# Kernel tuning notes

Hardware: AMD Instinct MI355X
Metric: run time of the kernel (lower is better)

## Reference

```python
import math
import jax, jax.numpy as jnp
import numpy as np

TWO_PI = 2.0 * math.pi


def make_coords(H, W):
    """Replicates ConvNet.generate_coordinates -> offsets of shape (9, 2, H, W).
    Pair k gives (dy, dx) for kernel tap k (row-major 3x3); center tap (k=4) is zero."""
    gy, gx = jnp.meshgrid(jnp.arange(H, dtype=jnp.float32),
                          jnp.arange(W, dtype=jnp.float32), indexing='ij')
    cy = H / 2.0 - 0.5
    cx = W / 2.0 - 0.5
    # torch: delta_x along height, delta_y along width; theta = atan2(dy, dx) mod 2pi
    theta = jnp.arctan2(gx - cx, gy - cy) % TWO_PI
    theta = jnp.round(theta * 10000.0) / 10000.0
    # per-tap (angle multiple m of pi/4, additive (ay, ax)); tap 4 (center) stays zero
    taps = [(0, 1.0, 1.0), (1, 1.0, 0.0), (2, 1.0, -1.0), (3, 0.0, 1.0), None,
            (4, 0.0, -1.0), (5, -1.0, 1.0), (6, -1.0, 0.0), (7, -1.0, -1.0)]
    offs = []
    zero = jnp.zeros_like(theta)
    for t in taps:
        if t is None:
            offs.append(jnp.stack([zero, zero]))
        else:
            m, ay, ax = t
            ang = theta + (math.pi / 4.0) * m
            offs.append(jnp.stack([jnp.cos(ang) + ay, jnp.sin(ang) + ax]))
    return jnp.stack(offs)  # (9, 2, H, W)


def deform_conv(x, off, w):
    """torchvision.ops.deform_conv2d, 3x3, stride 1, pad 1, dilation 1, no bias.
    x: (B,C,H,W), off: (9,2,H,W), w: (O,C,3,3) -> (B,O,H,W)."""
    B, C, H, W = x.shape
    ky = jnp.repeat(jnp.arange(3, dtype=jnp.float32), 3)  # (9,)
    kx = jnp.tile(jnp.arange(3, dtype=jnp.float32), 3)
    # sampling positions (H, W, 9)
    py = (jnp.arange(H, dtype=jnp.float32)[:, None, None] - 1.0
          + ky[None, None, :] + jnp.transpose(off[:, 0], (1, 2, 0)))
    px = (jnp.arange(W, dtype=jnp.float32)[None, :, None] - 1.0
          + kx[None, None, :] + jnp.transpose(off[:, 1], (1, 2, 0)))
    y0 = jnp.floor(py)
    x0 = jnp.floor(px)
    wy = py - y0  # bilinear weights
    wx = px - x0

    def gather(yf, xf):
        valid = (yf >= 0) & (yf <= H - 1) & (xf >= 0) & (xf <= W - 1)
        yi = jnp.clip(yf, 0, H - 1).astype(jnp.int32)
        xi = jnp.clip(xf, 0, W - 1).astype(jnp.int32)
        return x[:, :, yi, xi] * valid.astype(x.dtype)  # (B,C,H,W,9)

    sampled = ((1 - wy) * (1 - wx) * gather(y0, x0)
               + (1 - wy) * wx * gather(y0, x0 + 1)
               + wy * (1 - wx) * gather(y0 + 1, x0)
               + wy * wx * gather(y0 + 1, x0 + 1))
    return jnp.einsum('bchwk,ock->bohw', sampled, w.reshape(w.shape[0], C, 9))


def maxpool2(x):
    B, C, H, W = x.shape
    return x.reshape(B, C, H // 2, 2, W // 2, 2).max(axis=(3, 5))


def setup_inputs() -> dict:
    key = jax.random.key(0)
    ks = jax.random.split(key, 20)

    def kaiming(k, shape):
        fan_in = int(np.prod(shape[1:]))
        return jax.random.normal(k, shape, jnp.float32) * np.float32(np.sqrt(2.0 / fan_in))

    inp = {'x': jax.random.normal(ks[0], (8, 3, 128, 128), jnp.float32)}
    conv_shapes = [('w11', (64, 3, 3, 3)), ('w12', (64, 64, 3, 3)),
                   ('w21', (128, 64, 3, 3)), ('w22', (128, 128, 3, 3)),
                   ('w31', (256, 128, 3, 3)), ('w32', (256, 256, 3, 3)), ('w33', (256, 256, 3, 3)),
                   ('w41', (512, 256, 3, 3)), ('w42', (512, 512, 3, 3)), ('w43', (512, 512, 3, 3)),
                   ('w51', (512, 512, 3, 3)), ('w52', (512, 512, 3, 3)), ('w53', (512, 512, 3, 3))]
    for i, (n, s) in enumerate(conv_shapes):
        inp[n] = kaiming(ks[i + 1], s)
    inp['fc1_w'] = kaiming(ks[14], (4096, 512))
    inp['fc1_b'] = jnp.zeros((4096,), jnp.float32)
    inp['fc2_w'] = kaiming(ks[15], (4096, 4096))
    inp['fc2_b'] = jnp.zeros((4096,), jnp.float32)
    inp['fc3_w'] = kaiming(ks[16], (30, 4096))
    inp['fc3_b'] = jnp.zeros((30,), jnp.float32)
    return inp


def reference(x, w11, w12, w21, w22, w31, w32, w33, w41, w42, w43,
              w51, w52, w53, fc1_w, fc1_b, fc2_w, fc2_b, fc3_w, fc3_b):
    c128 = make_coords(128, 128)
    c64 = make_coords(64, 64)
    c32 = make_coords(32, 32)
    c16 = make_coords(16, 16)
    c8 = make_coords(8, 8)
    r = jax.nn.relu
    x = r(deform_conv(x, c128, w11))
    x = r(deform_conv(x, c128, w12))
    x = maxpool2(x)
    x = r(deform_conv(x, c64, w21))
    x = r(deform_conv(x, c64, w22))
    x = maxpool2(x)
    x = r(deform_conv(x, c32, w31))
    x = r(deform_conv(x, c32, w32))
    x = r(deform_conv(x, c32, w33))
    x = maxpool2(x)
    x = r(deform_conv(x, c16, w41))
    x = r(deform_conv(x, c16, w42))
    x = r(deform_conv(x, c16, w43))
    x = maxpool2(x)
    x = r(deform_conv(x, c8, w51))
    x = r(deform_conv(x, c8, w52))
    x = r(deform_conv(x, c8, w53))
    x = maxpool2(x)          # -> (B, 512, 4, 4)
    x = x.mean(axis=(2, 3))  # AvgPool2d((4,4)) on 4x4 -> (B, 512)
    x = r(x @ fc1_w.T + fc1_b)
    x = r(x @ fc2_w.T + fc2_b)
    return x @ fc3_w.T + fc3_b  # (B, 30)
```

## Files before the change

kernel.cpp:

```cpp
#include <hip/hip_runtime.h>
#include <math.h>

#define TWO_PI_F 6.283185307179586f
#define PI_4_F   0.7853981633974483f

typedef __attribute__((ext_vector_type(8))) short short8;
typedef __attribute__((ext_vector_type(4))) float f32x4;
typedef __attribute__((ext_vector_type(2))) float f32x2;
typedef __attribute__((ext_vector_type(4))) unsigned short ushort4v;
typedef __attribute__((ext_vector_type(4))) unsigned int uint4v;
typedef __attribute__((ext_vector_type(2))) unsigned int uint2v;

struct Tap { int i00, i01, i10, i11; float w00, w01, w10, w11; };

static __device__ __forceinline__ unsigned short f2bf(float f) {
    unsigned u = __builtin_bit_cast(unsigned, f);
    u = (u + 0x7fffu + ((u >> 16) & 1u)) >> 16;
    return (unsigned short)u;
}
static __device__ __forceinline__ float bf2f(unsigned short u) {
    return __builtin_bit_cast(float, (unsigned)u << 16);
}
static __device__ __forceinline__ f32x2 up2(unsigned u) {
    f32x2 r;
    r.x = __builtin_bit_cast(float, u << 16);
    r.y = __builtin_bit_cast(float, u & 0xffff0000u);
    return r;
}
static __device__ __forceinline__ unsigned cvt_pk_bf16(float lo, float hi) {
    unsigned r;
    asm("v_cvt_pk_bf16_f32 %0, %1, %2" : "=v"(r) : "v"(lo), "v"(hi));
    return r;
}

__global__ void build_table_kernel(Tap* __restrict__ tab, int* __restrict__ tabA, int S) {
    int idx = blockIdx.x * blockDim.x + threadIdx.x;
    int total = S * S * 9;
    if (idx >= total) return;
    int k = idx % 9;
    int p = idx / 9;
    int y = p / S;
    int x = p - y * S;
    int HW = S * S;

    float c = 0.5f * (float)S - 0.5f;
    float theta = atan2f((float)x - c, (float)y - c);
    theta = fmodf(theta, TWO_PI_F);
    if (theta < 0.0f) theta += TWO_PI_F;
    theta = rintf(theta * 10000.0f) / 10000.0f;

    float offy = 0.0f, offx = 0.0f;
    if (k != 4) {
        int m = (k < 4) ? k : (k - 1);
        const float ayt[8] = { 1.f, 1.f,  1.f, 0.f,  0.f, -1.f, -1.f, -1.f };
        const float axt[8] = { 1.f, 0.f, -1.f, 1.f, -1.f,  1.f,  0.f, -1.f };
        float ang = theta + PI_4_F * (float)m;
        offy = cosf(ang) + ayt[m];
        offx = sinf(ang) + axt[m];
    }
    int ky = k / 3, kx = k - ky * 3;
    float py = (float)y - 1.0f + (float)ky + offy;
    float px = (float)x - 1.0f + (float)kx + offx;
    float fy0 = floorf(py), fx0 = floorf(px);
    float wy = py - fy0, wx = px - fx0;
    float fmaxc = (float)(S - 1);

    Tap t;
    {
        float yy = fy0, xx = fx0;
        bool v = (yy >= 0.f) && (yy <= fmaxc) && (xx >= 0.f) && (xx <= fmaxc);
        int yi = (int)fminf(fmaxf(yy, 0.f), fmaxc);
        int xi = (int)fminf(fmaxf(xx, 0.f), fmaxc);
        t.i00 = yi * S + xi;
        t.w00 = v ? (1.f - wy) * (1.f - wx) : 0.f;
    }
    {
        float yy = fy0, xx = fx0 + 1.0f;
        bool v = (yy >= 0.f) && (yy <= fmaxc) && (xx >= 0.f) && (xx <= fmaxc);
        int yi = (int)fminf(fmaxf(yy, 0.f), fmaxc);
        int xi = (int)fminf(fmaxf(xx, 0.f), fmaxc);
        t.i01 = yi * S + xi;
        t.w01 = v ? (1.f - wy) * wx : 0.f;
    }
    {
        float yy = fy0 + 1.0f, xx = fx0;
        bool v = (yy >= 0.f) && (yy <= fmaxc) && (xx >= 0.f) && (xx <= fmaxc);
        int yi = (int)fminf(fmaxf(yy, 0.f), fmaxc);
        int xi = (int)fminf(fmaxf(xx, 0.f), fmaxc);
        t.i10 = yi * S + xi;
        t.w10 = v ? wy * (1.f - wx) : 0.f;
    }
    {
        float yy = fy0 + 1.0f, xx = fx0 + 1.0f;
        bool v = (yy >= 0.f) && (yy <= fmaxc) && (xx >= 0.f) && (xx <= fmaxc);
        int yi = (int)fminf(fmaxf(yy, 0.f), fmaxc);
        int xi = (int)fminf(fmaxf(xx, 0.f), fmaxc);
        t.i11 = yi * S + xi;
        t.w11 = v ? wy * wx : 0.f;
    }
    tab[idx] = t;

    int rec = (k * HW + p) * 8;
    tabA[rec + 0] = t.i00;
    tabA[rec + 1] = t.i01;
    tabA[rec + 2] = t.i10;
    tabA[rec + 3] = t.i11;
    tabA[rec + 4] = __builtin_bit_cast(int, t.w00);
    tabA[rec + 5] = __builtin_bit_cast(int, t.w01);
    tabA[rec + 6] = __builtin_bit_cast(int, t.w10);
    tabA[rec + 7] = __builtin_bit_cast(int, t.w11);
}

__global__ void pack_w_kernel(const float* __restrict__ w, unsigned short* __restrict__ wP,
                              int O, int C, int total) {
    int idx = blockIdx.x * blockDim.x + threadIdx.x;
    if (idx >= total) return;
    int ksub = idx & 31;
    int kbo  = idx >> 5;
    int o  = kbo % O;
    int kb = kbo / O;
    int K = kb * 32 + ksub;
    int kt = K / C;
    int c  = K - kt * C;
    wP[idx] = f2bf(w[((size_t)o * C + c) * 9 + kt]);
}

__global__ __launch_bounds__(256) void dconv_f32_kernel(
    const float* __restrict__ x, const float* __restrict__ w,
    const Tap* __restrict__ tab, unsigned short* __restrict__ out,
    int C, int O, int HW)
{
    __shared__ float4 sTabRaw[64 * 9 * 2];
    __shared__ float  sS[9][64];
    __shared__ float  sW[9][64];

    const int tid = threadIdx.x;
    const int b  = blockIdx.z;
    const int o0 = blockIdx.y * 64;
    const int p0 = blockIdx.x * 64;
    const int C9 = C * 9;

    const float4* gt = (const float4*)(tab + (size_t)p0 * 9);
    for (int i = tid; i < 64 * 9 * 2; i += 256) sTabRaw[i] = gt[i];
    const Tap* sTab = (const Tap*)sTabRaw;
    __syncthreads();

    float acc[4][4];
#pragma unroll
    for (int i = 0; i < 4; ++i)
#pragma unroll
        for (int j = 0; j < 4; ++j) acc[i][j] = 0.f;

    const int to = tid >> 4;
    const int tn = tid & 15;
    const float* xb = x + (size_t)b * C * HW;

    for (int c = 0; c < C; ++c) {
        const float* xp = xb + (size_t)c * HW;
        for (int i = tid; i < 9 * 64; i += 256) {
            int k = i >> 6;
            int p = i & 63;
            Tap t = sTab[p * 9 + k];
            sS[k][p] = t.w00 * xp[t.i00] + t.w01 * xp[t.i01]
                     + t.w10 * xp[t.i10] + t.w11 * xp[t.i11];
        }
        for (int i = tid; i < 9 * 64; i += 256) {
            int k = i >> 6;
            int o = i & 63;
            sW[k][o] = w[(size_t)(o0 + o) * C9 + c * 9 + k];
        }
        __syncthreads();
#pragma unroll
        for (int k = 0; k < 9; ++k) {
            float4 wv = *(const float4*)&sW[k][to * 4];
            float4 sv = *(const float4*)&sS[k][tn * 4];
            acc[0][0] += wv.x * sv.x; acc[0][1] += wv.x * sv.y; acc[0][2] += wv.x * sv.z; acc[0][3] += wv.x * sv.w;
            acc[1][0] += wv.y * sv.x; acc[1][1] += wv.y * sv.y; acc[1][2] += wv.y * sv.z; acc[1][3] += wv.y * sv.w;
            acc[2][0] += wv.z * sv.x; acc[2][1] += wv.z * sv.y; acc[2][2] += wv.z * sv.z; acc[2][3] += wv.z * sv.w;
            acc[3][0] += wv.w * sv.x; acc[3][1] += wv.w * sv.y; acc[3][2] += wv.w * sv.z; acc[3][3] += wv.w * sv.w;
        }
        __syncthreads();
    }

    const int ob   = (o0 + to * 4) >> 3;
    const int osub = (to & 1) << 2;
#pragma unroll
    for (int j = 0; j < 4; ++j) {
        int p = p0 + tn * 4 + j;
        ushort4v v;
        v.x = f2bf(fmaxf(acc[0][j], 0.f));
        v.y = f2bf(fmaxf(acc[1][j], 0.f));
        v.z = f2bf(fmaxf(acc[2][j], 0.f));
        v.w = f2bf(fmaxf(acc[3][j], 0.f));
        *(ushort4v*)(out + (((size_t)b * (O >> 3) + ob) * HW + p) * 8 + osub) = v;
    }
}

#define SPITCH 296

template<int BM>
__global__ __launch_bounds__(256, 4) void dconv_mfma(
    const unsigned short* __restrict__ x, const unsigned short* __restrict__ wP,
    const int* __restrict__ tabA, unsigned short* __restrict__ out,
    float* __restrict__ part,
    int C, int O, int HW, int Cchunk, int nChunks)
{
    __shared__ unsigned short sS[64 * SPITCH];

    const int tid  = threadIdx.x;
    const int lane = tid & 63;
    const int wv   = tid >> 6;
    const int bz = blockIdx.z;
    const int b     = bz & 7;
    const int chunk = bz >> 3;

    int bx = blockIdx.x;
    const int gx = gridDim.x;
    if ((gx & 7) == 0) { int g8 = gx >> 3; bx = (bx & 7) * g8 + (bx >> 3); }

    const int o0 = blockIdx.y * BM;
    const int p0 = bx * 64;
    const int c0 = chunk * Cchunk;
    const int nGroups = Cchunk >> 5;

    const int o0w = (BM == 128) ? wv * 32 : (wv >> 1) * 32;
    const int p0w = (BM == 128) ? 0       : (wv & 1) * 32;
    constexpr int MF = 2;
    constexpr int NF = (BM == 128) ? 4 : 2;

    f32x4 acc[MF][NF] = {};

    const unsigned short* xb = x + (size_t)b * C * HW;
    const int quad = lane >> 4;
    const int l16  = lane & 15;
    const int* tq = tabA + (((size_t)(p0 + lane)) << 3);
    unsigned short* srow = &sS[lane * SPITCH + (wv << 3)];

    for (int g = 0; g < nGroups; ++g) {
        const int cg = c0 + g * 32;
        const unsigned short* xcb = xb + ((((size_t)(cg >> 3) + wv) * HW) << 3);

#pragma unroll 3
        for (int kt = 0; kt < 9; ++kt) {
            const int* tp = tq + kt * (HW << 3);
            int4 ii = *(const int4*)tp;
            int4 iw = *(const int4*)(tp + 4);
            float w00 = __builtin_bit_cast(float, iw.x);
            float w01 = __builtin_bit_cast(float, iw.y);
            float w10 = __builtin_bit_cast(float, iw.z);
            float w11 = __builtin_bit_cast(float, iw.w);
            uint4v g00 = *(const uint4v*)(xcb + ((size_t)ii.x << 3));
            uint4v g01 = *(const uint4v*)(xcb + ((size_t)ii.y << 3));
            uint4v g10 = *(const uint4v*)(xcb + ((size_t)ii.z << 3));
            uint4v g11 = *(const uint4v*)(xcb + ((size_t)ii.w << 3));
            uint4v pk;
#pragma unroll
            for (int wd = 0; wd < 4; ++wd) {
                f32x2 s = up2(g00[wd]) * w00 + up2(g01[wd]) * w01
                        + up2(g10[wd]) * w10 + up2(g11[wd]) * w11;
                pk[wd] = cvt_pk_bf16(s.x, s.y);
            }
            *(uint4v*)(srow + kt * 32) = pk;
        }
        __syncthreads();

#pragma unroll 3
        for (int kt = 0; kt < 9; ++kt) {
            const int kb = (kt * C + cg) >> 5;
            short8 afr[MF], bfr[NF];
#pragma unroll
            for (int mf = 0; mf < MF; ++mf) {
                int orow = o0 + o0w + mf * 16 + l16;
                afr[mf] = *(const short8*)(wP + (((size_t)kb * O + orow) << 5) + (quad << 3));
            }
#pragma unroll
            for (int nf = 0; nf < NF; ++nf) {
                int prow = p0w + nf * 16 + l16;
                bfr[nf] = *(const short8*)(&sS[prow * SPITCH + kt * 32 + (quad << 3)]);
            }
#pragma unroll
            for (int mf = 0; mf < MF; ++mf)
#pragma unroll
                for (int nf = 0; nf < NF; ++nf)
                    acc[mf][nf] = __builtin_amdgcn_mfma_f32_16x16x32_bf16(afr[mf], bfr[nf], acc[mf][nf], 0, 0, 0);
        }
        __syncthreads();
    }

    const int O8 = O >> 3;
    if (nChunks == 1) {
#pragma unroll
        for (int mf = 0; mf < MF; ++mf)
#pragma unroll
            for (int nf = 0; nf < NF; ++nf) {
                int o = o0 + o0w + mf * 16 + (quad << 2);
                int p = p0 + p0w + nf * 16 + l16;
                size_t base = (((size_t)b * O8 + (o >> 3)) * HW + p) * 8 + (o & 7);
                uint2v pk2;
                pk2.x = cvt_pk_bf16(fmaxf(acc[mf][nf][0], 0.f), fmaxf(acc[mf][nf][1], 0.f));
                pk2.y = cvt_pk_bf16(fmaxf(acc[mf][nf][2], 0.f), fmaxf(acc[mf][nf][3], 0.f));
                *(uint2v*)(out + base) = pk2;
            }
    } else {
        float* pb = part + (size_t)chunk * 8 * O * HW;
#pragma unroll
        for (int mf = 0; mf < MF; ++mf)
#pragma unroll
            for (int nf = 0; nf < NF; ++nf) {
                int o = o0 + o0w + mf * 16 + (quad << 2);
                int p = p0 + p0w + nf * 16 + l16;
                size_t base = (((size_t)b * O8 + (o >> 3)) * HW + p) * 8 + (o & 7);
                *(f32x4*)(pb + base) = acc[mf][nf];
            }
    }
}

__global__ void reduce_relu_kernel(const float* __restrict__ part,
                                   unsigned short* __restrict__ out,
                                   int per4, int nChunks)
{
    int idx = blockIdx.x * blockDim.x + threadIdx.x;
    if (idx >= per4) return;
    const float4* p4 = (const float4*)part;
    float4 s = p4[idx];
    for (int ch = 1; ch < nChunks; ++ch) {
        float4 v = p4[(size_t)ch * per4 + idx];
        s.x += v.x; s.y += v.y; s.z += v.z; s.w += v.w;
    }
    ushort4v r;
    r.x = f2bf(fmaxf(s.x, 0.f)); r.y = f2bf(fmaxf(s.y, 0.f));
    r.z = f2bf(fmaxf(s.z, 0.f)); r.w = f2bf(fmaxf(s.w, 0.f));
    ((ushort4v*)out)[idx] = r;
}

__global__ void reduce_relu_pool_kernel(const float* __restrict__ part,
                                        unsigned short* __restrict__ out,
                                        int S, int per, int nChunks, int total)
{
    int idx = blockIdx.x * blockDim.x + threadIdx.x;
    if (idx >= total) return;
    int Sl = 31 - __clz(S);
    int W2 = S >> 1;
    int c8 = idx & 7;
    int t  = idx >> 3;
    int x2 = t & (W2 - 1); t >>= (Sl - 1);
    int y2 = t & (W2 - 1); t >>= (Sl - 1);
    size_t base = (((size_t)t * S + 2 * y2) * S + 2 * x2) * 8 + c8;
    size_t dX = 8;
    size_t dY = (size_t)S * 8;
    float s0 = 0.f, s1 = 0.f, s2 = 0.f, s3 = 0.f;
    for (int ch = 0; ch < nChunks; ++ch) {
        const float* p = part + (size_t)ch * per + base;
        s0 += p[0]; s1 += p[dX]; s2 += p[dY]; s3 += p[dY + dX];
    }
    out[idx] = f2bf(fmaxf(fmaxf(fmaxf(s0, s1), fmaxf(s2, s3)), 0.f));
}

__global__ void maxpool_kernel(const unsigned short* __restrict__ in,
                               unsigned short* __restrict__ out,
                               int S, int total)
{
    int idx = blockIdx.x * blockDim.x + threadIdx.x;
    if (idx >= total) return;
    int Sl = 31 - __clz(S);
    int W2 = S >> 1;
    int c8 = idx & 7;
    int t  = idx >> 3;
    int x2 = t & (W2 - 1); t >>= (Sl - 1);
    int y2 = t & (W2 - 1); t >>= (Sl - 1);
    size_t base = (((size_t)t * S + 2 * y2) * S + 2 * x2) * 8 + c8;
    size_t dY = (size_t)S * 8;
    const unsigned short* p = in + base;
    float m = fmaxf(fmaxf(bf2f(p[0]), bf2f(p[8])), fmaxf(bf2f(p[dY]), bf2f(p[dY + 8])));
    out[idx] = f2bf(m);
}

__global__ void avgpool_kernel(const unsigned short* __restrict__ in,
                               float* __restrict__ out, int total)
{
    int idx = blockIdx.x * blockDim.x + threadIdx.x;
    if (idx >= total) return;
    int b = idx >> 9;
    int c = idx & 511;
    int cb = c >> 3, c8 = c & 7;
    const unsigned short* p = in + (((size_t)(b * 64 + cb) * 16) << 3) + c8;
    float s = 0.f;
#pragma unroll
    for (int i = 0; i < 16; ++i) s += bf2f(p[i * 8]);
    out[idx] = s * (1.0f / 16.0f);
}

__global__ __launch_bounds__(256) void fc_kernel(
    const float* __restrict__ x, const float* __restrict__ w,
    const float* __restrict__ bias, float* __restrict__ out,
    int K, int O, int relu)
{
    int o = blockIdx.x;
    float acc[8] = {0.f,0.f,0.f,0.f,0.f,0.f,0.f,0.f};
    const float* wr = w + (size_t)o * K;
    for (int k = threadIdx.x; k < K; k += 256) {
        float wv = wr[k];
#pragma unroll
        for (int b = 0; b < 8; ++b) acc[b] += wv * x[(size_t)b * K + k];
    }
    __shared__ float red[8][256];
#pragma unroll
    for (int b = 0; b < 8; ++b) red[b][threadIdx.x] = acc[b];
    __syncthreads();
    for (int s = 128; s > 0; s >>= 1) {
        if (threadIdx.x < s) {
#pragma unroll
            for (int b = 0; b < 8; ++b) red[b][threadIdx.x] += red[b][threadIdx.x + s];
        }
        __syncthreads();
    }
    if (threadIdx.x < 8) {
        float v = red[threadIdx.x][0] + bias[o];
        if (relu) v = fmaxf(v, 0.f);
        out[(size_t)threadIdx.x * O + o] = v;
    }
}

extern "C" void kernel_launch(void* const* d_in, const int* in_sizes, int n_in,
                              void* d_out, int out_size, void* d_ws, size_t ws_size,
                              hipStream_t stream) {
    const float* x    = (const float*)d_in[0];
    const float* wf[13];
    for (int i = 0; i < 13; ++i) wf[i] = (const float*)d_in[1 + i];
    const float* fc1w = (const float*)d_in[14];
    const float* fc1b = (const float*)d_in[15];
    const float* fc2w = (const float*)d_in[16];
    const float* fc2b = (const float*)d_in[17];
    const float* fc3w = (const float*)d_in[18];
    const float* fc3b = (const float*)d_in[19];
    float* out = (float*)d_out;

    char* ws = (char*)d_ws;
    auto alloc = [&](size_t bytes) -> char* {
        char* p = ws;
        ws += (bytes + 255) & ~(size_t)255;
        return p;
    };

    const int sizes[5] = {128, 64, 32, 16, 8};
    Tap* tabs[5];
    int* tabAs[5];
    for (int i = 0; i < 5; ++i) {
        int HW = sizes[i] * sizes[i];
        tabs[i]  = (Tap*)alloc((size_t)HW * 9 * sizeof(Tap));
        tabAs[i] = (int*)alloc((size_t)HW * 9 * 8 * sizeof(int));
    }
    unsigned short* actA = (unsigned short*)alloc((size_t)8 * 64 * 128 * 128 * 2);
    unsigned short* actB = (unsigned short*)alloc((size_t)8 * 64 * 128 * 128 * 2);
    float* partial = (float*)alloc((size_t)2 * 8 * 128 * 4096 * sizeof(float));
    const int Cs[13] = {3, 64, 64, 128, 128, 256, 256, 256, 512, 512, 512, 512, 512};
    const int Os[13] = {64, 64, 128, 128, 256, 256, 256, 512, 512, 512, 512, 512, 512};
    unsigned short* wPk[13];
    wPk[0] = nullptr;
    for (int i = 1; i < 13; ++i)
        wPk[i] = (unsigned short*)alloc((size_t)Os[i] * Cs[i] * 9 * sizeof(unsigned short));
    float* pooled = (float*)alloc((size_t)8 * 512 * sizeof(float));
    float* fcb1 = (float*)alloc((size_t)8 * 4096 * sizeof(float));
    float* fcb2 = (float*)alloc((size_t)8 * 4096 * sizeof(float));

    for (int i = 0; i < 5; ++i) {
        int total = sizes[i] * sizes[i] * 9;
        build_table_kernel<<<(total + 255) / 256, 256, 0, stream>>>(tabs[i], tabAs[i], sizes[i]);
    }
    for (int i = 1; i < 13; ++i) {
        int total = Os[i] * Cs[i] * 9;
        pack_w_kernel<<<(total + 255) / 256, 256, 0, stream>>>(wf[i], wPk[i], Os[i], Cs[i], total);
    }

    auto convM = [&](const unsigned short* in, const unsigned short* wp, int* tabA,
                     unsigned short* o, int C, int O, int S, int nCh, bool leavePartial) {
        int HW = S * S;
        int Cchunk = C / nCh;
        if (O == 64) {
            dim3 grid(HW / 64, 1, 8 * nCh);
            dconv_mfma<64><<<grid, 256, 0, stream>>>(in, wp, tabA, o, partial, C, O, HW, Cchunk, nCh);
        } else {
            dim3 grid(HW / 64, O / 128, 8 * nCh);
            dconv_mfma<128><<<grid, 256, 0, stream>>>(in, wp, tabA, o, partial, C, O, HW, Cchunk, nCh);
        }
        if (nCh > 1 && !leavePartial) {
            int per4 = 8 * O * HW / 4;
            reduce_relu_kernel<<<(per4 + 255) / 256, 256, 0, stream>>>(partial, o, per4, nCh);
        }
    };
    auto fusedPool = [&](unsigned short* o, int C, int H, int nCh) {
        int per = 8 * C * H * H;
        int total = per / 4;
        reduce_relu_pool_kernel<<<(total + 255) / 256, 256, 0, stream>>>(partial, o, H, per, nCh, total);
    };

    {
        dim3 grid(128 * 128 / 64, 1, 8);
        dconv_f32_kernel<<<grid, 256, 0, stream>>>(x, wf[0], tabs[0], actA, 3, 64, 128 * 128);
    }
    convM(actA, wPk[1],  tabAs[0], actB, 64,  64,  128, 1, false);
    {
        int total = 8 * 64 * 64 * 64;
        maxpool_kernel<<<(total + 255) / 256, 256, 0, stream>>>(actB, actA, 128, total);
    }
    convM(actA, wPk[2],  tabAs[1], actB, 64,  128, 64, 2, false);
    convM(actB, wPk[3],  tabAs[1], nullptr, 128, 128, 64, 2, true);
    fusedPool(actA, 128, 64, 2);
    convM(actA, wPk[4],  tabAs[2], actB, 128, 256, 32, 2, false);
    convM(actB, wPk[5],  tabAs[2], actA, 256, 256, 32, 2, false);
    convM(actA, wPk[6],  tabAs[2], nullptr, 256, 256, 32, 2, true);
    fusedPool(actB, 256, 32, 2);
    convM(actB, wPk[7],  tabAs[3], actA, 256, 512, 16, 4, false);
    convM(actA, wPk[8],  tabAs[3], actB, 512, 512, 16, 4, false);
    convM(actB, wPk[9],  tabAs[3], nullptr, 512, 512, 16, 4, true);
    fusedPool(actA, 512, 16, 4);
    convM(actA, wPk[10], tabAs[4], actB, 512, 512, 8, 16, false);
    convM(actB, wPk[11], tabAs[4], actA, 512, 512, 8, 16, false);
    convM(actA, wPk[12], tabAs[4], nullptr, 512, 512, 8, 16, true);
    fusedPool(actB, 512, 8, 16);

    avgpool_kernel<<<(4096 + 255) / 256, 256, 0, stream>>>(actB, pooled, 8 * 512);

    fc_kernel<<<4096, 256, 0, stream>>>(pooled, fc1w, fc1b, fcb1, 512,  4096, 1);
    fc_kernel<<<4096, 256, 0, stream>>>(fcb1,   fc2w, fc2b, fcb2, 4096, 4096, 1);
    fc_kernel<<<30,   256, 0, stream>>>(fcb2,   fc3w, fc3b, out,  4096, 30,   0);
}
```

Baseline: 714.1 us.

## Replace LDS-staged deform conv with per-wave direct MFMA using split-bf16 precision

Rewrites the MFMA deformable-conv kernel so each wave gathers and bilinearly interpolates its own B fragments straight into registers, with no shared-memory staging and no block barriers. Weights and sampled activations are both split into bf16 hi/lo parts, and three MFMAs per tile reproduce near-fp32 accuracy. This triples the matrix work and doubles weight traffic. The per-layer chunking and pixel tile sizes also change: several 64x64 layers move to single chunk with 32-pixel tiles and a plain maxpool, and unused tap tables are no longer written. The change removes the LDS round-trip and sync cost in exchange for redundant gathers across waves and much more MFMA work.

```diff
diff --git a/kernel.cpp b/kernel.cpp
--- a/kernel.cpp
+++ b/kernel.cpp
@@ -9,7 +9,6 @@
 typedef __attribute__((ext_vector_type(2))) float f32x2;
 typedef __attribute__((ext_vector_type(4))) unsigned short ushort4v;
 typedef __attribute__((ext_vector_type(4))) unsigned int uint4v;
-typedef __attribute__((ext_vector_type(2))) unsigned int uint2v;
 
 struct Tap { int i00, i01, i10, i11; float w00, w01, w10, w11; };
 
@@ -98,7 +97,7 @@
         t.i11 = yi * S + xi;
         t.w11 = v ? wy * wx : 0.f;
     }
-    tab[idx] = t;
+    if (tab) tab[idx] = t;
 
     int rec = (k * HW + p) * 8;
     tabA[rec + 0] = t.i00;
@@ -111,7 +110,9 @@
     tabA[rec + 7] = __builtin_bit_cast(int, t.w11);
 }
 
-__global__ void pack_w_kernel(const float* __restrict__ w, unsigned short* __restrict__ wP,
+__global__ void pack_w_kernel(const float* __restrict__ w,
+                              unsigned short* __restrict__ wPhi,
+                              unsigned short* __restrict__ wPlo,
                               int O, int C, int total) {
     int idx = blockIdx.x * blockDim.x + threadIdx.x;
     if (idx >= total) return;
@@ -122,7 +123,10 @@
     int K = kb * 32 + ksub;
     int kt = K / C;
     int c  = K - kt * C;
-    wP[idx] = f2bf(w[((size_t)o * C + c) * 9 + kt]);
+    float wv = w[((size_t)o * C + c) * 9 + kt];
+    unsigned short h = f2bf(wv);
+    wPhi[idx] = h;
+    wPlo[idx] = f2bf(wv - bf2f(h));
 }
 
 __global__ __launch_bounds__(256) void dconv_f32_kernel(
@@ -196,119 +200,114 @@
     }
 }
 
-#define SPITCH 296
-
-template<int BM>
-__global__ __launch_bounds__(256, 4) void dconv_mfma(
-    const unsigned short* __restrict__ x, const unsigned short* __restrict__ wP,
+template<int NF>
+__global__ __launch_bounds__(256, 3) void dconv_direct(
+    const unsigned short* __restrict__ x,
+    const unsigned short* __restrict__ wPhi,
+    const unsigned short* __restrict__ wPlo,
     const int* __restrict__ tabA, unsigned short* __restrict__ out,
     float* __restrict__ part,
-    int C, int O, int HW, int Cchunk, int nChunks)
-{
-    __shared__ unsigned short sS[64 * SPITCH];
-
-    const int tid  = threadIdx.x;
-    const int lane = tid & 63;
-    const int wv   = tid >> 6;
-    const int bz = blockIdx.z;
-    const int b     = bz & 7;
-    const int chunk = bz >> 3;
+    int C, int O, int HW, int Cchunk, int nChunks, int nPx, int nO)
+{
+    const int lane = threadIdx.x & 63;
+    const int wv   = threadIdx.x >> 6;
 
     int bx = blockIdx.x;
     const int gx = gridDim.x;
     if ((gx & 7) == 0) { int g8 = gx >> 3; bx = (bx & 7) * g8 + (bx >> 3); }
 
-    const int o0 = blockIdx.y * BM;
-    const int p0 = bx * 64;
+    int wid = bx * 4 + wv;
+    const int ot = wid % nO;  wid /= nO;
+    const int px = wid % nPx; wid /= nPx;
+    const int b     = wid & 7;
+    const int chunk = wid >> 3;
+
+    const int o0 = ot * 64;
+    const int p0 = px * (NF * 16);
     const int c0 = chunk * Cchunk;
     const int nGroups = Cchunk >> 5;
 
-    const int o0w = (BM == 128) ? wv * 32 : (wv >> 1) * 32;
-    const int p0w = (BM == 128) ? 0       : (wv & 1) * 32;
-    constexpr int MF = 2;
-    constexpr int NF = (BM == 128) ? 4 : 2;
-
-    f32x4 acc[MF][NF] = {};
-
-    const unsigned short* xb = x + (size_t)b * C * HW;
     const int quad = lane >> 4;
     const int l16  = lane & 15;
-    const int* tq = tabA + (((size_t)(p0 + lane)) << 3);
-    unsigned short* srow = &sS[lane * SPITCH + (wv << 3)];
+
+    f32x4 acc[4][NF] = {};
+
+    const unsigned short* xb = x + (size_t)b * C * HW;
+    const int* tq = tabA + (((size_t)(p0 + l16)) << 3);
 
     for (int g = 0; g < nGroups; ++g) {
         const int cg = c0 + g * 32;
-        const unsigned short* xcb = xb + ((((size_t)(cg >> 3) + wv) * HW) << 3);
-
-#pragma unroll 3
-        for (int kt = 0; kt < 9; ++kt) {
-            const int* tp = tq + kt * (HW << 3);
-            int4 ii = *(const int4*)tp;
-            int4 iw = *(const int4*)(tp + 4);
-            float w00 = __builtin_bit_cast(float, iw.x);
-            float w01 = __builtin_bit_cast(float, iw.y);
-            float w10 = __builtin_bit_cast(float, iw.z);
-            float w11 = __builtin_bit_cast(float, iw.w);
-            uint4v g00 = *(const uint4v*)(xcb + ((size_t)ii.x << 3));
-            uint4v g01 = *(const uint4v*)(xcb + ((size_t)ii.y << 3));
-            uint4v g10 = *(const uint4v*)(xcb + ((size_t)ii.z << 3));
-            uint4v g11 = *(const uint4v*)(xcb + ((size_t)ii.w << 3));
-            uint4v pk;
-#pragma unroll
-            for (int wd = 0; wd < 4; ++wd) {
-                f32x2 s = up2(g00[wd]) * w00 + up2(g01[wd]) * w01
-                        + up2(g10[wd]) * w10 + up2(g11[wd]) * w11;
-                pk[wd] = cvt_pk_bf16(s.x, s.y);
-            }
-            *(uint4v*)(srow + kt * 32) = pk;
-        }
-        __syncthreads();
-
-#pragma unroll 3
+        const unsigned short* xq = xb + ((((size_t)(cg >> 3) + quad) * HW) << 3);
+
         for (int kt = 0; kt < 9; ++kt) {
             const int kb = (kt * C + cg) >> 5;
-            short8 afr[MF], bfr[NF];
-#pragma unroll
-            for (int mf = 0; mf < MF; ++mf) {
-                int orow = o0 + o0w + mf * 16 + l16;
-                afr[mf] = *(const short8*)(wP + (((size_t)kb * O + orow) << 5) + (quad << 3));
+            short8 ah[4], al[4];
+#pragma unroll
+            for (int mf = 0; mf < 4; ++mf) {
+                const size_t woff = (((size_t)kb * O + (o0 + mf * 16 + l16)) << 5) + (quad << 3);
+                ah[mf] = *(const short8*)(wPhi + woff);
+                al[mf] = *(const short8*)(wPlo + woff);
             }
+            const int* tk = tq + kt * (HW << 3);
 #pragma unroll
             for (int nf = 0; nf < NF; ++nf) {
-                int prow = p0w + nf * 16 + l16;
-                bfr[nf] = *(const short8*)(&sS[prow * SPITCH + kt * 32 + (quad << 3)]);
+                const int* tp = tk + (nf << 7);
+                int4 ii = *(const int4*)tp;
+                int4 iw = *(const int4*)(tp + 4);
+                float w00 = __builtin_bit_cast(float, iw.x);
+                float w01 = __builtin_bit_cast(float, iw.y);
+                float w10 = __builtin_bit_cast(float, iw.z);
+                float w11 = __builtin_bit_cast(float, iw.w);
+                uint4v g00 = *(const uint4v*)(xq + ((size_t)ii.x << 3));
+                uint4v g01 = *(const uint4v*)(xq + ((size_t)ii.y << 3));
+                uint4v g10 = *(const uint4v*)(xq + ((size_t)ii.z << 3));
+                uint4v g11 = *(const uint4v*)(xq + ((size_t)ii.w << 3));
+                uint4v ph, pl;
+#pragma unroll
+                for (int wd = 0; wd < 4; ++wd) {
+                    f32x2 s = up2(g00[wd]) * w00 + up2(g01[wd]) * w01
+                            + up2(g10[wd]) * w10 + up2(g11[wd]) * w11;
+                    unsigned h = cvt_pk_bf16(s.x, s.y);
+                    ph[wd] = h;
+                    f32x2 r = s - up2(h);
+                    pl[wd] = cvt_pk_bf16(r.x, r.y);
+                }
+                short8 bh = __builtin_bit_cast(short8, ph);
+                short8 bl = __builtin_bit_cast(short8, pl);
+#pragma unroll
+                for (int mf = 0; mf < 4; ++mf) {
+                    acc[mf][nf] = __builtin_amdgcn_mfma_f32_16x16x32_bf16(ah[mf], bh, acc[mf][nf], 0, 0, 0);
+                    acc[mf][nf] = __builtin_amdgcn_mfma_f32_16x16x32_bf16(ah[mf], bl, acc[mf][nf], 0, 0, 0);
+                    acc[mf][nf] = __builtin_amdgcn_mfma_f32_16x16x32_bf16(al[mf], bh, acc[mf][nf], 0, 0, 0);
+                }
             }
-#pragma unroll
-            for (int mf = 0; mf < MF; ++mf)
-#pragma unroll
-                for (int nf = 0; nf < NF; ++nf)
-                    acc[mf][nf] = __builtin_amdgcn_mfma_f32_16x16x32_bf16(afr[mf], bfr[nf], acc[mf][nf], 0, 0, 0);
-        }
-        __syncthreads();
+        }
     }
 
     const int O8 = O >> 3;
     if (nChunks == 1) {
 #pragma unroll
-        for (int mf = 0; mf < MF; ++mf)
+        for (int mf = 0; mf < 4; ++mf)
 #pragma unroll
             for (int nf = 0; nf < NF; ++nf) {
-                int o = o0 + o0w + mf * 16 + (quad << 2);
-                int p = p0 + p0w + nf * 16 + l16;
+                int o = o0 + mf * 16 + (quad << 2);
+                int p = p0 + nf * 16 + l16;
                 size_t base = (((size_t)b * O8 + (o >> 3)) * HW + p) * 8 + (o & 7);
-                uint2v pk2;
-                pk2.x = cvt_pk_bf16(fmaxf(acc[mf][nf][0], 0.f), fmaxf(acc[mf][nf][1], 0.f));
-                pk2.y = cvt_pk_bf16(fmaxf(acc[mf][nf][2], 0.f), fmaxf(acc[mf][nf][3], 0.f));
-                *(uint2v*)(out + base) = pk2;
+                ushort4v v;
+                v.x = f2bf(fmaxf(acc[mf][nf][0], 0.f));
+                v.y = f2bf(fmaxf(acc[mf][nf][1], 0.f));
+                v.z = f2bf(fmaxf(acc[mf][nf][2], 0.f));
+                v.w = f2bf(fmaxf(acc[mf][nf][3], 0.f));
+                *(ushort4v*)(out + base) = v;
             }
     } else {
         float* pb = part + (size_t)chunk * 8 * O * HW;
 #pragma unroll
-        for (int mf = 0; mf < MF; ++mf)
+        for (int mf = 0; mf < 4; ++mf)
 #pragma unroll
             for (int nf = 0; nf < NF; ++nf) {
-                int o = o0 + o0w + mf * 16 + (quad << 2);
-                int p = p0 + p0w + nf * 16 + l16;
+                int o = o0 + mf * 16 + (quad << 2);
+                int p = p0 + nf * 16 + l16;
                 size_t base = (((size_t)b * O8 + (o >> 3)) * HW + p) * 8 + (o & 7);
                 *(f32x4*)(pb + base) = acc[mf][nf];
             }
@@ -443,45 +442,52 @@
     };
 
     const int sizes[5] = {128, 64, 32, 16, 8};
-    Tap* tabs[5];
+    Tap* tab128 = (Tap*)alloc((size_t)128 * 128 * 9 * sizeof(Tap));
     int* tabAs[5];
     for (int i = 0; i < 5; ++i) {
         int HW = sizes[i] * sizes[i];
-        tabs[i]  = (Tap*)alloc((size_t)HW * 9 * sizeof(Tap));
         tabAs[i] = (int*)alloc((size_t)HW * 9 * 8 * sizeof(int));
     }
     unsigned short* actA = (unsigned short*)alloc((size_t)8 * 64 * 128 * 128 * 2);
     unsigned short* actB = (unsigned short*)alloc((size_t)8 * 64 * 128 * 128 * 2);
-    float* partial = (float*)alloc((size_t)2 * 8 * 128 * 4096 * sizeof(float));
+    float* partial = (float*)alloc((size_t)4 * 8 * 512 * 256 * sizeof(float));
     const int Cs[13] = {3, 64, 64, 128, 128, 256, 256, 256, 512, 512, 512, 512, 512};
     const int Os[13] = {64, 64, 128, 128, 256, 256, 256, 512, 512, 512, 512, 512, 512};
-    unsigned short* wPk[13];
-    wPk[0] = nullptr;
-    for (int i = 1; i < 13; ++i)
-        wPk[i] = (unsigned short*)alloc((size_t)Os[i] * Cs[i] * 9 * sizeof(unsigned short));
+    unsigned short* wPhi[13];
+    unsigned short* wPlo[13];
+    wPhi[0] = wPlo[0] = nullptr;
+    for (int i = 1; i < 13; ++i) {
+        wPhi[i] = (unsigned short*)alloc((size_t)Os[i] * Cs[i] * 9 * sizeof(unsigned short));
+        wPlo[i] = (unsigned short*)alloc((size_t)Os[i] * Cs[i] * 9 * sizeof(unsigned short));
+    }
     float* pooled = (float*)alloc((size_t)8 * 512 * sizeof(float));
     float* fcb1 = (float*)alloc((size_t)8 * 4096 * sizeof(float));
     float* fcb2 = (float*)alloc((size_t)8 * 4096 * sizeof(float));
 
     for (int i = 0; i < 5; ++i) {
         int total = sizes[i] * sizes[i] * 9;
-        build_table_kernel<<<(total + 255) / 256, 256, 0, stream>>>(tabs[i], tabAs[i], sizes[i]);
+        build_table_kernel<<<(total + 255) / 256, 256, 0, stream>>>(
+            (i == 0) ? tab128 : nullptr, tabAs[i], sizes[i]);
     }
     for (int i = 1; i < 13; ++i) {
         int total = Os[i] * Cs[i] * 9;
-        pack_w_kernel<<<(total + 255) / 256, 256, 0, stream>>>(wf[i], wPk[i], Os[i], Cs[i], total);
-    }
-
-    auto convM = [&](const unsigned short* in, const unsigned short* wp, int* tabA,
-                     unsigned short* o, int C, int O, int S, int nCh, bool leavePartial) {
+        pack_w_kernel<<<(total + 255) / 256, 256, 0, stream>>>(wf[i], wPhi[i], wPlo[i], Os[i], Cs[i], total);
+    }
+
+    auto convM = [&](const unsigned short* in, int li,
+                     unsigned short* o, int C, int O, int S, int nCh, int NP, bool leavePartial) {
         int HW = S * S;
         int Cchunk = C / nCh;
-        if (O == 64) {
-            dim3 grid(HW / 64, 1, 8 * nCh);
-            dconv_mfma<64><<<grid, 256, 0, stream>>>(in, wp, tabA, o, partial, C, O, HW, Cchunk, nCh);
+        int nPx = HW / NP;
+        int nO  = O / 64;
+        int waves = nPx * nO * 8 * nCh;
+        int tabIdx = (S == 128) ? 0 : (S == 64) ? 1 : (S == 32) ? 2 : (S == 16) ? 3 : 4;
+        if (NP == 64) {
+            dconv_direct<4><<<dim3(waves / 4), 256, 0, stream>>>(
+                in, wPhi[li], wPlo[li], tabAs[tabIdx], o, partial, C, O, HW, Cchunk, nCh, nPx, nO);
         } else {
-            dim3 grid(HW / 64, O / 128, 8 * nCh);
-            dconv_mfma<128><<<grid, 256, 0, stream>>>(in, wp, tabA, o, partial, C, O, HW, Cchunk, nCh);
+            dconv_direct<2><<<dim3(waves / 4), 256, 0, stream>>>(
+                in, wPhi[li], wPlo[li], tabAs[tabIdx], o, partial, C, O, HW, Cchunk, nCh, nPx, nO);
         }
         if (nCh > 1 && !leavePartial) {
             int per4 = 8 * O * HW / 4;
@@ -493,33 +499,34 @@
         int total = per / 4;
         reduce_relu_pool_kernel<<<(total + 255) / 256, 256, 0, stream>>>(partial, o, H, per, nCh, total);
     };
+    auto pool = [&](const unsigned short* in, unsigned short* o, int C, int S) {
+        int total = 8 * C * (S / 2) * (S / 2);
+        maxpool_kernel<<<(total + 255) / 256, 256, 0, stream>>>(in, o, S, total);
+    };
 
     {
         dim3 grid(128 * 128 / 64, 1, 8);
-        dconv_f32_kernel<<<grid, 256, 0, stream>>>(x, wf[0], tabs[0], actA, 3, 64, 128 * 128);
-    }
-    convM(actA, wPk[1],  tabAs[0], actB, 64,  64,  128, 1, false);
-    {
-        int total = 8 * 64 * 64 * 64;
-        maxpool_kernel<<<(total + 255) / 256, 256, 0, stream>>>(actB, actA, 128, total);
-    }
-    convM(actA, wPk[2],  tabAs[1], actB, 64,  128, 64, 2, false);
-    convM(actB, wPk[3],  tabAs[1], nullptr, 128, 128, 64, 2, true);
-    fusedPool(actA, 128, 64, 2);
-    convM(actA, wPk[4],  tabAs[2], actB, 128, 256, 32, 2, false);
-    convM(actB, wPk[5],  tabAs[2], actA, 256, 256, 32, 2, false);
-    convM(actA, wPk[6],  tabAs[2], nullptr, 256, 256, 32, 2, true);
-    fusedPool(actB, 256, 32, 2);
-    convM(actB, wPk[7],  tabAs[3], actA, 256, 512, 16, 4, false);
-    convM(actA, wPk[8],  tabAs[3], actB, 512, 512, 16, 4, false);
-    convM(actB, wPk[9],  tabAs[3], nullptr, 512, 512, 16, 4, true);
-    fusedPool(actA, 512, 16, 4);
-    convM(actA, wPk[10], tabAs[4], actB, 512, 512, 8, 16, false);
-    convM(actB, wPk[11], tabAs[4], actA, 512, 512, 8, 16, false);
-    convM(actA, wPk[12], tabAs[4], nullptr, 512, 512, 8, 16, true);
-    fusedPool(actB, 512, 8, 16);
-
-    avgpool_kernel<<<(4096 + 255) / 256, 256, 0, stream>>>(actB, pooled, 8 * 512);
+        dconv_f32_kernel<<<grid, 256, 0, stream>>>(x, wf[0], tab128, actA, 3, 64, 128 * 128);
+    }
+    convM(actA, 1,  actB, 64,  64,  128, 1, 64, false);
+    pool(actB, actA, 64, 128);
+    convM(actA, 2,  actB, 64,  128, 64, 1, 32, false);
+    convM(actB, 3,  actA, 128, 128, 64, 1, 32, false);
+    pool(actA, actB, 128, 64);
+    convM(actB, 4,  actA, 128, 256, 32, 2, 64, false);
+    convM(actA, 5,  actB, 256, 256, 32, 2, 64, false);
+    convM(actB, 6,  nullptr, 256, 256, 32, 2, 64, true);
+    fusedPool(actA, 256, 32, 2);
+    convM(actA, 7,  actB, 256, 512, 16, 4, 64, false);
+    convM(actB, 8,  actA, 512, 512, 16, 4, 64, false);
+    convM(actA, 9,  nullptr, 512, 512, 16, 4, 64, true);
+    fusedPool(actB, 512, 16, 4);
+    convM(actB, 10, actA, 512, 512, 8, 16, 64, false);
+    convM(actA, 11, actB, 512, 512, 8, 16, 64, false);
+    convM(actB, 12, nullptr, 512, 512, 8, 16, 64, true);
+    fusedPool(actA, 512, 8, 16);
+
+    avgpool_kernel<<<(4096 + 255) / 256, 256, 0, stream>>>(actA, pooled, 8 * 512);
 
     fc_kernel<<<4096, 256, 0, stream>>>(pooled, fc1w, fc1b, fcb1, 512,  4096, 1);
     fc_kernel<<<4096, 256, 0, stream>>>(fcb1,   fc2w, fc2b, fcb2, 4096, 4096, 1);
```

After: 1.082 ms. 1.52x slower.
